# Performance work log

Measured on AMD Instinct MI355X. Metric: run time of the kernel, lower is better.

The kernel has to match this reference:

```python
import jax, jax.numpy as jnp
from jax import lax
import numpy as np


def conv2d(x, w, b=None, stride=1, pad=0, groups=1):
    out = lax.conv_general_dilated(x, w, (stride, stride), [(pad, pad), (pad, pad)],
                                   dimension_numbers=('NCHW', 'OIHW', 'NCHW'),
                                   feature_group_count=groups)
    if b is not None:
        out = out + b[None, :, None, None]
    return out


def ln(x, g, b, eps=1e-5):
    m = x.mean(-1, keepdims=True)
    v = ((x - m) ** 2).mean(-1, keepdims=True)
    return (x - m) * lax.rsqrt(v + eps) * g + b


def grid_sample_bilinear(img, grid):
    # img [N,C,H,W]; grid [N,Hg,Wg,2] with (x,y) in [-1,1]; align_corners=True, zeros padding
    N, C, H, W = img.shape
    x = (grid[..., 0] + 1.0) * 0.5 * (W - 1)
    y = (grid[..., 1] + 1.0) * 0.5 * (H - 1)
    x0 = jnp.floor(x); y0 = jnp.floor(y)
    x1 = x0 + 1.0; y1 = y0 + 1.0
    wx1 = x - x0; wx0 = 1.0 - wx1
    wy1 = y - y0; wy0 = 1.0 - wy1
    imgh = img.transpose(0, 2, 3, 1)  # [N,H,W,C]
    bidx = jnp.arange(N)[:, None, None]
    def g(ix, iy):
        valid = (ix >= 0) & (ix <= W - 1) & (iy >= 0) & (iy <= H - 1)
        ixc = jnp.clip(ix, 0, W - 1).astype(jnp.int32)
        iyc = jnp.clip(iy, 0, H - 1).astype(jnp.int32)
        return imgh[bidx, iyc, ixc] * valid[..., None].astype(img.dtype)
    out = (g(x0, y0) * (wx0 * wy0)[..., None] + g(x1, y0) * (wx1 * wy0)[..., None]
           + g(x0, y1) * (wx0 * wy1)[..., None] + g(x1, y1) * (wx1 * wy1)[..., None])
    return out.transpose(0, 3, 1, 2)  # [N,C,Hg,Wg]


def setup_inputs() -> dict:
    key = jax.random.key(0)
    ks = iter(jax.random.split(key, 64))
    def rn(shape, s=0.02):
        return jax.random.normal(next(ks), shape, jnp.float32) * s
    B, C, H, W = 4, 512, 32, 32
    gc, hid = 256, 1024
    d = {}
    d['feat_tgt'] = jax.random.normal(next(ks), (B, C, H, W), jnp.float32)
    d['feat_ref'] = jax.random.normal(next(ks), (B, C, H, W), jnp.float32)
    d['emb_w'] = rn((C, 2 * C, 3, 3)); d['emb_b'] = jnp.zeros((C,), jnp.float32)
    d['q_w'] = rn((C, C)); d['q_b'] = jnp.zeros((C,), jnp.float32)
    d['k_w'] = rn((C, C)); d['k_b'] = jnp.zeros((C,), jnp.float32)
    d['v_w'] = rn((C, C)); d['v_b'] = jnp.zeros((C,), jnp.float32)
    d['out_w'] = rn((C, C)); d['out_b'] = jnp.zeros((C,), jnp.float32)
    d['ln1_w'] = jnp.ones((gc,), jnp.float32); d['ln1_b'] = jnp.zeros((gc,), jnp.float32)
    d['mb_n1_w'] = jnp.ones((gc,), jnp.float32); d['mb_n1_b'] = jnp.zeros((gc,), jnp.float32)
    d['mb_q_w'] = rn((gc, gc)); d['mb_q_b'] = jnp.zeros((gc,), jnp.float32)
    d['mb_kv_w'] = rn((2 * gc, gc)); d['mb_kv_b'] = jnp.zeros((2 * gc,), jnp.float32)
    d['mb_proj_w'] = rn((gc, gc)); d['mb_proj_b'] = jnp.zeros((gc,), jnp.float32)
    d['mb_n2_w'] = jnp.ones((gc,), jnp.float32); d['mb_n2_b'] = jnp.zeros((gc,), jnp.float32)
    d['mb_fc1_w'] = rn((hid, gc)); d['mb_fc1_b'] = jnp.zeros((hid,), jnp.float32)
    d['mb_dw_w'] = rn((hid, 1, 3, 3)); d['mb_dw_b'] = jnp.zeros((hid,), jnp.float32)
    d['mb_fc2_w'] = rn((gc, hid)); d['mb_fc2_b'] = jnp.zeros((gc,), jnp.float32)
    d['co_dw_w'] = rn((gc, 1, 9, 9)); d['co_dw_b'] = jnp.zeros((gc,), jnp.float32)
    d['co_ln_w'] = jnp.ones((gc,), jnp.float32); d['co_ln_b'] = jnp.zeros((gc,), jnp.float32)
    d['co_out_w'] = rn((2, gc))
    return d


def reference(feat_tgt, feat_ref, emb_w, emb_b, q_w, q_b, k_w, k_b, v_w, v_b, out_w, out_b,
              ln1_w, ln1_b, mb_n1_w, mb_n1_b, mb_q_w, mb_q_b, mb_kv_w, mb_kv_b,
              mb_proj_w, mb_proj_b, mb_n2_w, mb_n2_b, mb_fc1_w, mb_fc1_b, mb_dw_w, mb_dw_b,
              mb_fc2_w, mb_fc2_b, co_dw_w, co_dw_b, co_ln_w, co_ln_b, co_out_w):
    B, C, H, W = feat_tgt.shape
    G = 2                      # n_groups
    gc = C // G                # n_group_channels
    heads, hc = 8, C // 8      # n_heads, n_head_channels
    # embedding conv over concat(target, reference)
    feat = conv2d(jnp.concatenate([feat_tgt, feat_ref], 1), emb_w, emb_b, pad=1)
    q = jnp.einsum('bchw,oc->bohw', feat_tgt, q_w) + q_b[None, :, None, None]
    # group tokens + LN
    fg = feat.reshape(B * G, gc, H * W).transpose(0, 2, 1)  # [BG, N, gc]
    x = ln(fg, ln1_w, ln1_b)
    # ---- MitBlock offset generator ----
    BG, N, D = x.shape
    mh = 8; mhd = D // mh
    h = ln(x, mb_n1_w, mb_n1_b, 1e-6)
    qq = (h @ mb_q_w.T + mb_q_b).reshape(BG, N, mh, mhd).transpose(0, 2, 1, 3)
    kv = (h @ mb_kv_w.T + mb_kv_b).reshape(BG, N, 2, mh, mhd).transpose(2, 0, 3, 1, 4)
    kk, vv = kv[0], kv[1]
    a = jax.nn.softmax(jnp.einsum('bhnd,bhmd->bhnm', qq, kk) * (mhd ** -0.5), axis=-1)
    o = jnp.einsum('bhnm,bhmd->bhnd', a, vv).transpose(0, 2, 1, 3).reshape(BG, N, D)
    x = x + (o @ mb_proj_w.T + mb_proj_b)
    h2 = ln(x, mb_n2_w, mb_n2_b, 1e-6)
    m = h2 @ mb_fc1_w.T + mb_fc1_b                         # [BG, N, hid]
    hid = m.shape[-1]
    mi = m.transpose(0, 2, 1).reshape(BG, hid, H, W)
    mi = conv2d(mi, mb_dw_w, mb_dw_b, pad=1, groups=hid)
    m = jax.nn.gelu(mi.reshape(BG, hid, N).transpose(0, 2, 1), approximate=False)
    x = x + (m @ mb_fc2_w.T + mb_fc2_b)
    # ---- conv_offset stack ----
    off = x.reshape(BG, H, W, gc).transpose(0, 3, 1, 2)
    off = conv2d(off, co_dw_w, co_dw_b, pad=4, groups=gc)
    off = ln(off.transpose(0, 2, 3, 1), co_ln_w, co_ln_b).transpose(0, 3, 1, 2)
    off = jax.nn.gelu(off, approximate=False)
    off = jnp.einsum('bchw,oc->bohw', off, co_out_w)       # [BG, 2, Hk, Wk]
    Hk, Wk = off.shape[2], off.shape[3]
    ns = Hk * Wk
    rng = jnp.array([1.0 / Hk, 1.0 / Wk], feat.dtype).reshape(1, 2, 1, 1)
    off = jnp.tanh(off) * rng * 2.0                        # offset_range_factor = 2
    off = off.transpose(0, 2, 3, 1)                        # [BG, Hk, Wk, 2] (y,x)
    ry = (jnp.linspace(0.5, Hk - 0.5, Hk, dtype=feat.dtype) / Hk) * 2 - 1
    rx = (jnp.linspace(0.5, Wk - 0.5, Wk, dtype=feat.dtype) / Wk) * 2 - 1
    ref = jnp.stack(jnp.meshgrid(ry, rx, indexing='ij'), -1)  # [Hk, Wk, 2] (y,x)
    pos = off + ref[None]
    sampled = grid_sample_bilinear(feat.reshape(BG, gc, H, W), pos[..., ::-1])
    sampled = sampled.reshape(B, C, ns)
    k = jnp.einsum('bcn,oc->bon', sampled, k_w) + k_b[None, :, None]
    v = jnp.einsum('bcn,oc->bon', sampled, v_w) + v_b[None, :, None]
    qh = q.reshape(B * heads, hc, H * W)
    kh = k.reshape(B * heads, hc, ns)
    vh = v.reshape(B * heads, hc, ns)
    attn = jax.nn.softmax(jnp.einsum('bcm,bcn->bmn', qh, kh) * (hc ** -0.5), axis=-1)
    out = jnp.einsum('bmn,bcn->bcm', attn, vh).reshape(B, C, H, W)
    y = jnp.einsum('bchw,oc->bohw', out, out_w) + out_b[None, :, None, None]
    return y
```

## Files before the change

### kernel.cpp

```cpp
#include <hip/hip_runtime.h>
#include <math.h>


static constexpr int HW = 1024;

typedef __attribute__((ext_vector_type(8))) short bf16x8;
typedef __attribute__((ext_vector_type(4))) float f32x4;

union V16u { int4 i4; ushort u[8]; };

__device__ __forceinline__ float gelu_exact(float v) {
  return 0.5f * v * (1.0f + erff(v * 0.7071067811865475f));
}

__device__ __forceinline__ ushort bf16_rne(float v) {
  unsigned int b = __float_as_uint(v);
  return (ushort)((b + 0x7fffu + ((b >> 16) & 1u)) >> 16);
}

__device__ __forceinline__ void split2(float v, ushort& h, ushort& l) {
  h = bf16_rne(v);
  l = bf16_rne(v - __uint_as_float(((unsigned int)h) << 16));
}

__device__ __forceinline__ void wfrag_body(const float* __restrict__ W, int K, int KC,
                                           ushort* __restrict__ dh, ushort* __restrict__ dl,
                                           int gtid) {
  int l = gtid & 63; int fr = gtid >> 6;
  int kc = fr % KC; int ot = fr / KC;
  int lr = l & 15, lu = l >> 4;
  const float* sp = W + (size_t)(ot * 16 + lr) * K + kc * 32 + lu * 8;
  V16u hi, lo;
#pragma unroll
  for (int j = 0; j < 8; ++j) split2(sp[j], hi.u[j], lo.u[j]);
  *(int4*)(dh + (size_t)gtid * 8) = hi.i4;
  *(int4*)(dl + (size_t)gtid * 8) = lo.i4;
}

__global__ void k_prep_all(
    const float* __restrict__ emb_w, const float* __restrict__ tgt,
    const float* __restrict__ refp,
    const float* q_w, const float* k_w, const float* v_w, const float* o_w,
    const float* mq_w, const float* mkv_w, const float* mp_w,
    const float* f1_w, const float* f2_w, const float* dw9_w,
    const float* mq_b, const float* mkv_b, const float* k_b, const float* v_b,
    ushort* __restrict__ WtEH, ushort* __restrict__ WtEL,
    ushort* __restrict__ XtH, ushort* __restrict__ XtL,
    ushort* qh, ushort* ql, ushort* kvh, ushort* kvl,
    ushort* oh, ushort* ol, ushort* mqkvh, ushort* mqkvl,
    ushort* mph, ushort* mpl, ushort* f1h, ushort* f1l, ushort* f2h, ushort* f2l,
    float* wt9, float* biasmb, float* biaskv) {
  int bid = blockIdx.x, tid = threadIdx.x;
  if (bid < 2048) {
    int idx = bid * 256 + tid;
    int o = idx >> 10, ci = idx & 1023;
    const float* src = emb_w + (size_t)idx * 9;
#pragma unroll
    for (int t = 0; t < 9; ++t) {
      ushort h, l; split2(src[t], h, l);
      size_t oo = ((size_t)(t * 512 + o)) * 1024 + ci;
      WtEH[oo] = h; WtEL[oo] = l;
    }
  } else if (bid < 4360) {
    int idx = (bid - 2048) * 256 + tid;
    int xp = idx % 34; int r = idx / 34;
    int g8 = r & 127; r >>= 7;
    int yp = r % 34; int b = r / 34;
    int y = yp - 1, x = xp - 1;
    bool valid = (unsigned)y < 32u && (unsigned)x < 32u;
    V16u hi, lo;
    const float* in = (g8 < 64) ? (tgt + ((size_t)(b * 512 + g8 * 8)) * HW)
                                : (refp + ((size_t)(b * 512 + (g8 - 64) * 8)) * HW);
#pragma unroll
    for (int j = 0; j < 8; ++j) {
      float v = valid ? in[(size_t)j * HW + y * 32 + x] : 0.f;
      split2(v, hi.u[j], lo.u[j]);
    }
    size_t oo = (((size_t)(b * 34 + yp)) * 34 + xp) * 1024 + g8 * 8;
    *(int4*)(XtH + oo) = hi.i4;
    *(int4*)(XtL + oo) = lo.i4;
  }
  else if (bid < 4488) wfrag_body(q_w, 512, 16, qh, ql, (bid - 4360) * 256 + tid);
  else if (bid < 4616) wfrag_body(k_w, 512, 16, kvh, kvl, (bid - 4488) * 256 + tid);
  else if (bid < 4744) wfrag_body(v_w, 512, 16, kvh + 262144, kvl + 262144,
                                  (bid - 4616) * 256 + tid);
  else if (bid < 4872) wfrag_body(o_w, 512, 16, oh, ol, (bid - 4744) * 256 + tid);
  else if (bid < 4904) wfrag_body(mq_w, 256, 8, mqkvh, mqkvl, (bid - 4872) * 256 + tid);
  else if (bid < 4968) wfrag_body(mkv_w, 256, 8, mqkvh + 65536, mqkvl + 65536,
                                  (bid - 4904) * 256 + tid);
  else if (bid < 5000) wfrag_body(mp_w, 256, 8, mph, mpl, (bid - 4968) * 256 + tid);
  else if (bid < 5128) wfrag_body(f1_w, 256, 8, f1h, f1l, (bid - 5000) * 256 + tid);
  else if (bid < 5256) wfrag_body(f2_w, 1024, 32, f2h, f2l, (bid - 5128) * 256 + tid);
  else if (bid < 5337) {
    int idx = (bid - 5256) * 256 + tid;
    int t = idx >> 8, c = idx & 255;
    wt9[idx] = dw9_w[c * 81 + t];
  } else {
    int idx = (bid - 5337) * 256 + tid;
    if (idx < 768) biasmb[idx] = idx < 256 ? mq_b[idx] : mkv_b[idx - 256];
    else if (idx < 1792) {
      int j = idx - 768;
      biaskv[j] = j < 512 ? k_b[j] : v_b[j - 512];
    }
  }
}

__global__ void k_prep_cm2frag(const float* __restrict__ src, int CH, int KC,
                               ushort* __restrict__ dh, ushort* __restrict__ dl) {
  int gtid = blockIdx.x * 256 + threadIdx.x;
  int l = gtid & 63; int fr = gtid >> 6;
  int kc = fr % KC; int r2 = fr / KC; int nt = r2 & 63; int b = r2 >> 6;
  int lr = l & 15, lu = l >> 4;
  const float* sp = src + ((size_t)(b * CH) + kc * 32 + lu * 8) * 1024 + nt * 16 + lr;
  V16u hi, lo;
#pragma unroll
  for (int j = 0; j < 8; ++j) split2(sp[(size_t)j * 1024], hi.u[j], lo.u[j]);
  *(int4*)(dh + (size_t)gtid * 8) = hi.i4;
  *(int4*)(dl + (size_t)gtid * 8) = lo.i4;
}

__global__ __launch_bounds__(256, 2)
void k_emb_mfma(const ushort* __restrict__ Xt_hi, const ushort* __restrict__ Xt_lo,
                const ushort* __restrict__ Wt_hi, const ushort* __restrict__ Wt_lo,
                float* __restrict__ part) {
  int wgid = (blockIdx.x & 7) * 64 + (blockIdx.x >> 3);
  int yt = wgid & 7;  wgid >>= 3;
  int b  = wgid & 3;  wgid >>= 2;
  int mt = wgid & 3;  wgid >>= 2;
  int ks = wgid;
  int tid = threadIdx.x;
  int w = tid >> 6, l = tid & 63;
  int lr = l & 15, lu = l >> 4;
  int y0 = yt * 4;
  int obase = mt * 128 + w * 32;

  __shared__ int4 LsH[2][816];
  __shared__ int4 LsL[2][816];

  int4 gh[4], gl[4];
  int kc0 = ks * 8;

  auto loadstage = [&](int kcg) {
#pragma unroll
    for (int i = 0; i < 4; ++i) {
      int s = tid + 256 * i;
      if (s < 816) {
        int px = s >> 2;
        int u = (s & 3) ^ ((px >> 1) & 3);
        size_t off = ((size_t)(b * 34 + y0) * 34 + px) * 1024 + kcg * 32 + u * 8;
        gh[i] = *(const int4*)(Xt_hi + off);
        gl[i] = *(const int4*)(Xt_lo + off);
      }
    }
  };
  auto writestage = [&](int buf) {
// ... 112 lines not shown
void k_gemm_mfma(const ushort* __restrict__ Ah, const ushort* __restrict__ Al,
                 const ushort* __restrict__ Bh, const ushort* __restrict__ Bl,
                 const float* __restrict__ bias, float* __restrict__ Y,
                 int KC, int MT, int Mtot) {
  int bid = blockIdx.x;
  int ntb = bid & 15; bid >>= 4;
  int mt = bid % MT; int b = bid / MT;
  int tid = threadIdx.x, w = tid >> 6, l = tid & 63, lr = l & 15, lu = l >> 4;
  int wo = w >> 1, wn = w & 1;
  int ot0 = mt * 4 + wo * 2;
  int nf0 = ntb * 4 + wn * 2;
  const bf16x8* pAh = (const bf16x8*)Ah;
  const bf16x8* pAl = (const bf16x8*)Al;
  const bf16x8* pBh = (const bf16x8*)Bh;
  const bf16x8* pBl = (const bf16x8*)Bl;
  f32x4 zero = {0.f, 0.f, 0.f, 0.f};
  f32x4 acc[2][2];
#pragma unroll
  for (int a = 0; a < 2; ++a)
#pragma unroll
    for (int n = 0; n < 2; ++n) acc[a][n] = zero;
  for (int kc = 0; kc < KC; ++kc) {
    bf16x8 a_h[2], a_l[2];
#pragma unroll
    for (int a = 0; a < 2; ++a) {
      size_t idx = ((size_t)(ot0 + a) * KC + kc) * 64 + l;
      a_h[a] = pAh[idx]; a_l[a] = pAl[idx];
    }
#pragma unroll
    for (int n = 0; n < 2; ++n) {
      size_t idx = (((size_t)(b * 64 + nf0 + n)) * KC + kc) * 64 + l;
      bf16x8 b_h = pBh[idx], b_l = pBl[idx];
#pragma unroll
      for (int a = 0; a < 2; ++a) {
        acc[a][n] = __builtin_amdgcn_mfma_f32_16x16x32_bf16(a_h[a], b_h, acc[a][n], 0, 0, 0);
        acc[a][n] = __builtin_amdgcn_mfma_f32_16x16x32_bf16(a_h[a], b_l, acc[a][n], 0, 0, 0);
        acc[a][n] = __builtin_amdgcn_mfma_f32_16x16x32_bf16(a_l[a], b_h, acc[a][n], 0, 0, 0);
      }
    }
  }
#pragma unroll
  for (int a = 0; a < 2; ++a) {
    int o = (ot0 + a) * 16 + lu * 4;
#pragma unroll
    for (int n = 0; n < 2; ++n) {
      int col = (nf0 + n) * 16 + lr;
#pragma unroll
      for (int r = 0; r < 4; ++r)
        Y[((size_t)(b * Mtot + o + r)) * 1024 + col] = acc[a][n][r] + bias[o + r];
    }
  }
}

__global__ void k_transadd_tm(const float* __restrict__ Pcm, float* __restrict__ Xtm) {
  __shared__ float T[64][65];
  int bid = blockIdx.x; int n0 = (bid & 15) << 6; bid >>= 4;
  int c0 = (bid & 3) << 6; int bg = bid >> 2;
  int cl = threadIdx.x & 63, rw = threadIdx.x >> 6;
#pragma unroll
  for (int i = 0; i < 16; ++i) {
    int crow = i * 4 + rw;
    T[crow][cl] = Pcm[((size_t)(bg * 256 + c0 + crow)) * 1024 + n0 + cl];
  }
  __syncthreads();
#pragma unroll
  for (int i = 0; i < 16; ++i) {
    int nrow = i * 4 + rw;
    Xtm[((size_t)((bg << 10) + n0 + nrow)) * 256 + c0 + cl] += T[cl][nrow];
  }
}

__global__ void k_transadd_nc(const float* __restrict__ Yg, const float* __restrict__ Xtm,
                              float* __restrict__ out_nc) {
  __shared__ float T[64][65];
  int bid = blockIdx.x; int n0 = (bid & 15) << 6; bid >>= 4;
  int c0 = (bid & 3) << 6; int bg = bid >> 2;
  int cl = threadIdx.x & 63, rw = threadIdx.x >> 6;
#pragma unroll
  for (int i = 0; i < 16; ++i) {
    int crow = i * 4 + rw;
    T[crow][cl] = Yg[((size_t)(bg * 256 + c0 + crow)) * 1024 + n0 + cl];
  }
  __syncthreads();
#pragma unroll
  for (int i = 0; i < 16; ++i) {
    int nrow = i * 4 + rw;
    size_t a = ((size_t)((bg << 10) + n0 + nrow)) * 256 + c0 + cl;
    out_nc[a] = T[cl][nrow] + Xtm[a];
  }
}

__global__ void k_ln1n1(const float* __restrict__ featnc,
                        const float* __restrict__ g1, const float* __restrict__ b1,
                        const float* __restrict__ gn, const float* __restrict__ bn,
                        float* __restrict__ xbuf,
                        ushort* __restrict__ dh, ushort* __restrict__ dl) {
  int token = (blockIdx.x * 256 + threadIdx.x) >> 6;
  int lane = threadIdx.x & 63;
  float4 v4 = *reinterpret_cast<const float4*>(featnc + (size_t)token * 256 + lane * 4);
  float s  = v4.x + v4.y + v4.z + v4.w;
  float s2 = v4.x * v4.x + v4.y * v4.y + v4.z * v4.z + v4.w * v4.w;
#pragma unroll
  for (int off = 32; off; off >>= 1) { s += __shfl_xor(s, off); s2 += __shfl_xor(s2, off); }
  float mean = s * (1.f / 256.f);
  float rstd = rsqrtf(s2 * (1.f / 256.f) - mean * mean + 1e-5f);
  float4 g4 = *reinterpret_cast<const float4*>(g1 + lane * 4);
  float4 b4 = *reinterpret_cast<const float4*>(b1 + lane * 4);
  float4 x;
  x.x = (v4.x - mean) * rstd * g4.x + b4.x;
  x.y = (v4.y - mean) * rstd * g4.y + b4.y;
  x.z = (v4.z - mean) * rstd * g4.z + b4.z;
  x.w = (v4.w - mean) * rstd * g4.w + b4.w;
  *reinterpret_cast<float4*>(xbuf + (size_t)token * 256 + lane * 4) = x;
  float t  = x.x + x.y + x.z + x.w;
  float t2 = x.x * x.x + x.y * x.y + x.z * x.z + x.w * x.w;
#pragma unroll
  for (int off = 32; off; off >>= 1) { t += __shfl_xor(t, off); t2 += __shfl_xor(t2, off); }
  float mean2 = t * (1.f / 256.f);
  float rstd2 = rsqrtf(t2 * (1.f / 256.f) - mean2 * mean2 + 1e-6f);
  float4 gg = *reinterpret_cast<const float4*>(gn + lane * 4);
  float4 bb = *reinterpret_cast<const float4*>(bn + lane * 4);
  ushort4 h4, l4;
  split2((x.x - mean2) * rstd2 * gg.x + bb.x, h4.x, l4.x);
  split2((x.y - mean2) * rstd2 * gg.y + bb.y, h4.y, l4.y);
  split2((x.z - mean2) * rstd2 * gg.z + bb.z, h4.z, l4.z);
  split2((x.w - mean2) * rstd2 * gg.w + bb.w, h4.w, l4.w);
  int bg = token >> 10, nt = (token >> 4) & 63, lr = token & 15;
  int kc = lane >> 3, lu_f = (lane >> 1) & 3, j0 = (lane & 1) * 4;
  size_t base = ((((size_t)(bg * 64 + nt)) * 8 + kc) * 64 + lu_f * 16 + lr) * 8 + j0;
  *(ushort4*)(dh + base) = h4;
  *(ushort4*)(dl + base) = l4;
}

__global__ void k_ln_frag(const float* __restrict__ xin, const float* __restrict__ g_,
                          const float* __restrict__ b_, ushort* __restrict__ dh,
                          ushort* __restrict__ dl, float eps) {
  int token = (blockIdx.x * 256 + threadIdx.x) >> 6;
  int lane = threadIdx.x & 63;
  float4 v4 = *reinterpret_cast<const float4*>(xin + (size_t)token * 256 + lane * 4);
  float s  = v4.x + v4.y + v4.z + v4.w;
  float s2 = v4.x * v4.x + v4.y * v4.y + v4.z * v4.z + v4.w * v4.w;
#pragma unroll
  for (int off = 32; off; off >>= 1) { s += __shfl_xor(s, off); s2 += __shfl_xor(s2, off); }
  float mean = s * (1.f / 256.f);
  float rstd = rsqrtf(s2 * (1.f / 256.f) - mean * mean + eps);
  float4 g4 = *reinterpret_cast<const float4*>(g_ + lane * 4);
  float4 b4 = *reinterpret_cast<const float4*>(b_ + lane * 4);
  ushort4 h4, l4;
  split2((v4.x - mean) * rstd * g4.x + b4.x, h4.x, l4.x);
  split2((v4.y - mean) * rstd * g4.y + b4.y, h4.y, l4.y);
  split2((v4.z - mean) * rstd * g4.z + b4.z, h4.z, l4.z);
  split2((v4.w - mean) * rstd * g4.w + b4.w, h4.w, l4.w);
  int bg = token >> 10, nt = (token >> 4) & 63, lr = token & 15;
  int kc = lane >> 3, lu_f = (lane >> 1) & 3, j0 = (lane & 1) * 4;
  size_t base = ((((size_t)(bg * 64 + nt)) * 8 + kc) * 64 + lu_f * 16 + lr) * 8 + j0;
  *(ushort4*)(dh + base) = h4;
  *(ushort4*)(dl + base) = l4;
}

__global__ void k_prep_mb3(const float* __restrict__ qkv,
                           ushort* __restrict__ mQh, ushort* __restrict__ mQl,
                           ushort* __restrict__ mKh, ushort* __restrict__ mKl,
                           ushort* __restrict__ mVh, ushort* __restrict__ mVl) {
  int bid = blockIdx.x, tid = threadIdx.x;
  int sect = bid >> 10, lb = bid & 1023;
  int gtid = lb * 256 + tid;
  int l = gtid & 63; int fr = gtid >> 6;
  int lr = l & 15, lu = l >> 4;
  V16u hi, lo;
  if (sect < 2) {
    int nt = fr & 63; int bgh = fr >> 6;
    int bg = bgh >> 3, hh = bgh & 7;
    int rowbase = sect == 0 ? 0 : 256;
    float scale = sect == 0 ? 0.17677669529663689f : 1.f;
    const float* sp = qkv + ((size_t)(bg * 768 + rowbase + hh * 32 + lu * 8)) * 1024
                      + nt * 16 + lr;
#pragma unroll
    for (int j = 0; j < 8; ++j) split2(sp[(size_t)j * 1024] * scale, hi.u[j], lo.u[j]);
    ushort* dh = sect == 0 ? mQh : mKh;
    ushort* dl = sect == 0 ? mQl : mKl;
    *(int4*)(dh + (size_t)gtid * 8) = hi.i4;
    *(int4*)(dl + (size_t)gtid * 8) = lo.i4;
  } else {
    int kc = fr & 31; int et = (fr >> 5) & 1; int bgh = fr >> 6;
    int bg = bgh >> 3, hh = bgh & 7;
    const float* sp = qkv + ((size_t)(bg * 768 + 512 + hh * 32 + et * 16 + lr)) * 1024
                      + kc * 32 + lu * 8;
#pragma unroll
    for (int j = 0; j < 8; ++j) split2(sp[j], hi.u[j], lo.u[j]);
    *(int4*)(mVh + (size_t)gtid * 8) = hi.i4;
    *(int4*)(mVl + (size_t)gtid * 8) = lo.i4;
  }
}

__global__ void k_prep_main3(const float* __restrict__ qb, const float* __restrict__ kv2,
                             ushort* __restrict__ aQh, ushort* __restrict__ aQl,
                             ushort* __restrict__ aKh, ushort* __restrict__ aKl,
                             ushort* __restrict__ aVh, ushort* __restrict__ aVl) {
  int bid = blockIdx.x, tid = threadIdx.x;
  int sect = bid >> 10, lb = bid & 1023;
  int gtid = lb * 256 + tid;
  int l = gtid & 63, tile = gtid >> 6;
  int lr = l & 15, lu = l >> 4;
  V16u hi, lo;
  if (sect < 2) {
    int dc = tile & 1, nt = (tile >> 1) & 63, bh = tile >> 7;
    int b = bh >> 3, h = bh & 7;
    const float* sp;
    float scale;
    if (sect == 0) {
      scale = 0.125f;
      sp = qb + ((size_t)(b * 512 + h * 64 + dc * 32 + lu * 8)) * 1024 + nt * 16 + lr;
    } else {
      scale = 1.f;
      sp = kv2 + ((size_t)(b * 1024 + h * 64 + dc * 32 + lu * 8)) * 1024 + nt * 16 + lr;
    }
#pragma unroll
    for (int j = 0; j < 8; ++j) split2(sp[(size_t)j * 1024] * scale, hi.u[j], lo.u[j]);
    ushort* dh = sect == 0 ? aQh : aKh;
    ushort* dl = sect == 0 ? aQl : aKl;
    *(int4*)(dh + (size_t)gtid * 8) = hi.i4;
    *(int4*)(dl + (size_t)gtid * 8) = lo.i4;
  } else {
    int kc = tile & 31, et = (tile >> 5) & 3, bh = tile >> 7;
    int b = bh >> 3, h = bh & 7;
    const float* sp = kv2 + ((size_t)(b * 1024 + 512 + h * 64 + et * 16 + lr)) * 1024
                      + kc * 32 + lu * 8;
#pragma unroll
    for (int j = 0; j < 8; ++j) split2(sp[j], hi.u[j], lo.u[j]);
    *(int4*)(aVh + (size_t)gtid * 8) = hi.i4;
    *(int4*)(aVl + (size_t)gtid * 8) = lo.i4;
  }
}

__global__ __launch_bounds__(256)
void k_mbattn_mfma(const ushort* __restrict__ Qh, const ushort* __restrict__ Ql,
                   const ushort* __restrict__ Kh, const ushort* __restrict__ Kl,
                   const ushort* __restrict__ Vh, const ushort* __restrict__ Vl,
                   ushort* __restrict__ ofh, ushort* __restrict__ ofl) {
  int qb = blockIdx.x & 15, bgh = blockIdx.x >> 4;
  int tid = threadIdx.x, w = tid >> 6, l = tid & 63, lr = l & 15, lu = l >> 4;
  int qt = qb * 4 + w;
  bf16x8 qh = ((const bf16x8*)Qh)[(size_t)(bgh * 64 + qt) * 64 + l];
  bf16x8 ql = ((const bf16x8*)Ql)[(size_t)(bgh * 64 + qt) * 64 + l];
  __shared__ ushort Ph[4][16][72];
  __shared__ ushort Pl[4][16][72];
  f32x4 zero = {0.f, 0.f, 0.f, 0.f};
  f32x4 oacc[2] = {zero, zero};
  float den = 0.f;
  for (int kb = 0; kb < 16; ++kb) {
#pragma unroll
    for (int kt4 = 0; kt4 < 4; ++kt4) {
      int kt = kb * 4 + kt4;
      bf16x8 kh = ((const bf16x8*)Kh)[(size_t)(bgh * 64 + kt) * 64 + l];
      bf16x8 kl = ((const bf16x8*)Kl)[(size_t)(bgh * 64 + kt) * 64 + l];
      f32x4 s = zero;
      s = __builtin_amdgcn_mfma_f32_16x16x32_bf16(kh, qh, s, 0, 0, 0);
      s = __builtin_amdgcn_mfma_f32_16x16x32_bf16(kh, ql, s, 0, 0, 0);
      s = __builtin_amdgcn_mfma_f32_16x16x32_bf16(kl, qh, s, 0, 0, 0);
      uint2 uh, ul;
      {
        float p0 = __expf(s[0]), p1 = __expf(s[1]), p2 = __expf(s[2]), p3 = __expf(s[3]);
        den += (p0 + p1) + (p2 + p3);
        ushort h0, l0, h1, l1, h2, l2, h3, l3;
        split2(p0, h0, l0); split2(p1, h1, l1); split2(p2, h2, l2); split2(p3, h3, l3);
        uh.x = (unsigned)h0 | ((unsigned)h1 << 16); uh.y = (unsigned)h2 | ((unsigned)h3 << 16);
        ul.x = (unsigned)l0 | ((unsigned)l1 << 16); ul.y = (unsigned)l2 | ((unsigned)l3 << 16);
      }
      *(uint2*)&Ph[w][lr][kt4 * 16 + lu * 4] = uh;
      *(uint2*)&Pl[w][lr][kt4 * 16 + lu * 4] = ul;
    }
#pragma unroll
    for (int kc2 = 0; kc2 < 2; ++kc2) {
      int kc = kb * 2 + kc2;
      bf16x8 bph = *(const bf16x8*)&Ph[w][lr][kc2 * 32 + lu * 8];
      bf16x8 bpl = *(const bf16x8*)&Pl[w][lr][kc2 * 32 + lu * 8];
#pragma unroll
      for (int et = 0; et < 2; ++et) {
        bf16x8 vh = ((const bf16x8*)Vh)[(size_t)((bgh * 2 + et) * 32 + kc) * 64 + l];
        bf16x8 vl = ((const bf16x8*)Vl)[(size_t)((bgh * 2 + et) * 32 + kc) * 64 + l];
        oacc[et] = __builtin_amdgcn_mfma_f32_16x16x32_bf16(vh, bph, oacc[et], 0, 0, 0);
        oacc[et] = __builtin_amdgcn_mfma_f32_16x16x32_bf16(vh, bpl, oacc[et], 0, 0, 0);
        oacc[et] = __builtin_amdgcn_mfma_f32_16x16x32_bf16(vl, bph, oacc[et], 0, 0, 0);
      }
    }
// ... 210 lines not shown
  }
  __syncthreads();
  const float* src = Xnc + (size_t)(bg << 10) * 256;
  for (int n = 0; n < 64; ++n) {
    float acc = src[(size_t)sI[0][n] * 256 + tid] * sW[0][n]
              + src[(size_t)sI[1][n] * 256 + tid] * sW[1][n]
              + src[(size_t)sI[2][n] * 256 + tid] * sW[2][n]
              + src[(size_t)sI[3][n] * 256 + tid] * sW[3][n];
    out_nc[((size_t)((bg << 10) + nch * 64 + n)) * 256 + tid] = acc;
  }
}

extern "C" void kernel_launch(void* const* d_in, const int* in_sizes, int n_in,
                              void* d_out, int out_size, void* d_ws, size_t ws_size,
                              hipStream_t stream) {
  const float* tgt    = (const float*)d_in[0];
  const float* refp   = (const float*)d_in[1];
  const float* emb_w  = (const float*)d_in[2];
  const float* emb_b  = (const float*)d_in[3];
  const float* q_w    = (const float*)d_in[4];
  const float* q_b    = (const float*)d_in[5];
  const float* k_w    = (const float*)d_in[6];
  const float* k_b    = (const float*)d_in[7];
  const float* v_w    = (const float*)d_in[8];
  const float* v_b    = (const float*)d_in[9];
  const float* out_w  = (const float*)d_in[10];
  const float* out_b  = (const float*)d_in[11];
  const float* ln1_w  = (const float*)d_in[12];
  const float* ln1_b  = (const float*)d_in[13];
  const float* n1_w   = (const float*)d_in[14];
  const float* n1_b   = (const float*)d_in[15];
  const float* mbq_w  = (const float*)d_in[16];
  const float* mbq_b  = (const float*)d_in[17];
  const float* mbkv_w = (const float*)d_in[18];
  const float* mbkv_b = (const float*)d_in[19];
  const float* mbp_w  = (const float*)d_in[20];
  const float* mbp_b  = (const float*)d_in[21];
  const float* n2_w   = (const float*)d_in[22];
  const float* n2_b   = (const float*)d_in[23];
  const float* fc1_w  = (const float*)d_in[24];
  const float* fc1_b  = (const float*)d_in[25];
  const float* dw3_w  = (const float*)d_in[26];
  const float* dw3_b  = (const float*)d_in[27];
  const float* fc2_w  = (const float*)d_in[28];
  const float* fc2_b  = (const float*)d_in[29];
  const float* dw9_w  = (const float*)d_in[30];
  const float* dw9_b  = (const float*)d_in[31];
  const float* coln_w = (const float*)d_in[32];
  const float* coln_b = (const float*)d_in[33];
  const float* coout_w= (const float*)d_in[34];

  float* ws = (float*)d_ws;
  float* slabA = ws + 0;
  float* qbuf  = ws + 2097152;
  float* xbuf  = ws + 4194304;
  float* slabD = ws + 6291456;
  float* slabE = ws + 8388608;
  float* slabF = ws + 10485760;
  float* slabG = ws + 14680064;
  float* slabH = ws + 23068672;
  float* featnc= ws + 31457280;
  float* posb  = ws + 35389440;
  float* wt9   = ws + 35405824;
  float* biasmb= ws + 35426560;
  float* biaskv= ws + 35427328;

  ushort* XtH = (ushort*)(ws + 4194304);
  ushort* XtL = XtH + 4734976;
  ushort* WtEH = (ushort*)slabG;
  ushort* WtEL = WtEH + 4718592;
  float* part = slabH;
  ushort* tgtfh = (ushort*)slabF;
  ushort* tgtfl = tgtfh + 2097152;

  ushort* J = (ushort*)(ws + 33554432);
  ushort* wfq_h   = J;                ushort* wfq_l   = J + 262144;
  ushort* wfkv_h  = J + 524288;       ushort* wfkv_l  = J + 1048576;
  ushort* wfo_h   = J + 1572864;      ushort* wfo_l   = J + 1835008;
  ushort* wfmqkv_h= J + 2097152;      ushort* wfmqkv_l= J + 2293760;
  ushort* wfmp_h  = J + 2490368;      ushort* wfmp_l  = J + 2555904;
  ushort* wff1_h  = J + 2621440;      ushort* wff1_l  = J + 2883584;
  ushort* wff2_h  = J + 3145728;      ushort* wff2_l  = J + 3407872;

  ushort* hfh = (ushort*)slabG;     ushort* hfl = hfh + 2097152;
  float* qkv_cm = slabE;
  ushort* mQh = (ushort*)slabG;     ushort* mQl = mQh + 2097152;
  ushort* mKh = mQh + 4194304;      ushort* mKl = mQh + 6291456;
  ushort* mVh = mQh + 8388608;      ushort* mVl = mQh + 10485760;
  ushort* ofh = (ushort*)slabF;     ushort* ofl = ofh + 2097152;
  float* P_cm = slabD;
  ushort* h2fh = (ushort*)slabF;    ushort* h2fl = h2fh + 2097152;
  float* m_cm = slabG;
  float* mi_cm = slabH;
  ushort* mifh = (ushort*)slabG;    ushort* mifl = mifh + 8388608;
  float* ygemm = slabD;
  float* offin = slabA;
  float* offdwnc = slabE;
  float* samplednc = slabA;
  ushort* sfh = (ushort*)slabF;     ushort* sfl = sfh + 2097152;
  float* kv2 = slabD;
  ushort* aQh = (ushort*)slabG;     ushort* aQl = aQh + 2097152;
  ushort* aKh = aQh + 4194304;      ushort* aKl = aQh + 6291456;
  ushort* aVh = aQh + 8388608;      ushort* aVl = aQh + 10485760;
  ushort* anfh = (ushort*)slabH;    ushort* anfl = anfh + 2097152;

  k_prep_all<<<5344, 256, 0, stream>>>(
      emb_w, tgt, refp, q_w, k_w, v_w, out_w, mbq_w, mbkv_w, mbp_w, fc1_w, fc2_w,
      dw9_w, mbq_b, mbkv_b, k_b, v_b,
      WtEH, WtEL, XtH, XtL,
      wfq_h, wfq_l, wfkv_h, wfkv_l, wfo_h, wfo_l, wfmqkv_h, wfmqkv_l,
      wfmp_h, wfmp_l, wff1_h, wff1_l, wff2_h, wff2_l,
      wt9, biasmb, biaskv);
  k_prep_cm2frag<<<1024, 256, 0, stream>>>(tgt, 512, 16, tgtfh, tgtfl);
  k_emb_mfma<<<512, 256, 0, stream>>>(XtH, XtL, WtEH, WtEL, part);
  k_embmerge_nc<<<512, 256, 0, stream>>>(part, emb_b, featnc);
  k_gemm_mfma<<<512, 256, 0, stream>>>(wfq_h, wfq_l, tgtfh, tgtfl, q_b, qbuf, 16, 8, 512);
  k_ln1n1<<<2048, 256, 0, stream>>>(featnc, ln1_w, ln1_b, n1_w, n1_b, xbuf, hfh, hfl);
  k_gemm_mfma<<<1536, 256, 0, stream>>>(wfmqkv_h, wfmqkv_l, hfh, hfl, biasmb, qkv_cm, 8, 12, 768);
  k_prep_mb3<<<3072, 256, 0, stream>>>(qkv_cm, mQh, mQl, mKh, mKl, mVh, mVl);
  k_mbattn_mfma<<<1024, 256, 0, stream>>>(mQh, mQl, mKh, mKl, mVh, mVl, ofh, ofl);
  k_gemm_mfma<<<512, 256, 0, stream>>>(wfmp_h, wfmp_l, ofh, ofl, mbp_b, P_cm, 8, 4, 256);
  k_transadd_tm<<<512, 256, 0, stream>>>(P_cm, xbuf);
  k_ln_frag<<<2048, 256, 0, stream>>>(xbuf, n2_w, n2_b, h2fh, h2fl, 1e-6f);
  k_gemm_mfma<<<2048, 256, 0, stream>>>(wff1_h, wff1_l, h2fh, h2fl, fc1_b, m_cm, 8, 16, 1024);
  k_dw3<<<32768, 256, 0, stream>>>(m_cm, dw3_w, dw3_b, mi_cm);
  k_prep_cm2frag<<<4096, 256, 0, stream>>>(mi_cm, 1024, 32, mifh, mifl);
  k_gemm_mfma<<<512, 256, 0, stream>>>(wff2_h, wff2_l, mifh, mifl, fc2_b, ygemm, 32, 4, 256);
  k_transadd_nc<<<512, 256, 0, stream>>>(ygemm, xbuf, offin);
  k_dw9_nc<<<1024, 256, 0, stream>>>(offin, wt9, dw9_b, offdwnc);
  k_cotail_nc<<<2048, 256, 0, stream>>>(offdwnc, coln_w, coln_b, coout_w, posb);
  k_gsample_nc<<<128, 256, 0, stream>>>(featnc, posb, samplednc);
  k_prep_s2frag<<<1024, 256, 0, stream>>>(samplednc, sfh, sfl);
  k_gemm_mfma<<<1024, 256, 0, stream>>>(wfkv_h, wfkv_l, sfh, sfl, biaskv, kv2, 16, 16, 1024);
  k_prep_main3<<<3072, 256, 0, stream>>>(qbuf, kv2, aQh, aQl, aKh, aKl, aVh, aVl);
  k_mainattn_mfma<<<512, 256, 0, stream>>>(aQh, aQl, aKh, aKl, aVh, aVl, anfh, anfl);
  k_gemm_mfma<<<512, 256, 0, stream>>>(wfo_h, wfo_l, anfh, anfl, out_b, (float*)d_out, 16, 8, 512);
}
```

Before: 591.5 us.

## Fuse Q/K/V fragment packing into GEMM epilogues and fold attention scale into weights

Result: faster. 575.7 us (-2.7%).

```diff
diff --git a/kernel.cpp b/kernel.cpp
--- a/kernel.cpp
+++ b/kernel.cpp
@@ -25,14 +25,14 @@
 
 __device__ __forceinline__ void wfrag_body(const float* __restrict__ W, int K, int KC,
                                            ushort* __restrict__ dh, ushort* __restrict__ dl,
-                                           int gtid) {
+                                           int gtid, float scale) {
   int l = gtid & 63; int fr = gtid >> 6;
   int kc = fr % KC; int ot = fr / KC;
   int lr = l & 15, lu = l >> 4;
   const float* sp = W + (size_t)(ot * 16 + lr) * K + kc * 32 + lu * 8;
   V16u hi, lo;
 #pragma unroll
-  for (int j = 0; j < 8; ++j) split2(sp[j], hi.u[j], lo.u[j]);
+  for (int j = 0; j < 8; ++j) split2(sp[j] * scale, hi.u[j], lo.u[j]);
   *(int4*)(dh + (size_t)gtid * 8) = hi.i4;
   *(int4*)(dl + (size_t)gtid * 8) = lo.i4;
 }
@@ -43,13 +43,14 @@
     const float* q_w, const float* k_w, const float* v_w, const float* o_w,
     const float* mq_w, const float* mkv_w, const float* mp_w,
     const float* f1_w, const float* f2_w, const float* dw9_w,
-    const float* mq_b, const float* mkv_b, const float* k_b, const float* v_b,
+    const float* q_b, const float* mq_b, const float* mkv_b,
+    const float* k_b, const float* v_b,
     ushort* __restrict__ WtEH, ushort* __restrict__ WtEL,
     ushort* __restrict__ XtH, ushort* __restrict__ XtL,
     ushort* qh, ushort* ql, ushort* kvh, ushort* kvl,
     ushort* oh, ushort* ol, ushort* mqkvh, ushort* mqkvl,
     ushort* mph, ushort* mpl, ushort* f1h, ushort* f1l, ushort* f2h, ushort* f2l,
-    float* wt9, float* biasmb, float* biaskv) {
+    float* wt9, float* biasmb, float* biaskv, float* biasq) {
   int bid = blockIdx.x, tid = threadIdx.x;
   if (bid < 2048) {
     int idx = bid * 256 + tid;
@@ -80,27 +81,31 @@
     *(int4*)(XtH + oo) = hi.i4;
     *(int4*)(XtL + oo) = lo.i4;
   }
-  else if (bid < 4488) wfrag_body(q_w, 512, 16, qh, ql, (bid - 4360) * 256 + tid);
-  else if (bid < 4616) wfrag_body(k_w, 512, 16, kvh, kvl, (bid - 4488) * 256 + tid);
+  else if (bid < 4488) wfrag_body(q_w, 512, 16, qh, ql, (bid - 4360) * 256 + tid, 0.125f);
+  else if (bid < 4616) wfrag_body(k_w, 512, 16, kvh, kvl, (bid - 4488) * 256 + tid, 1.f);
   else if (bid < 4744) wfrag_body(v_w, 512, 16, kvh + 262144, kvl + 262144,
-                                  (bid - 4616) * 256 + tid);
-  else if (bid < 4872) wfrag_body(o_w, 512, 16, oh, ol, (bid - 4744) * 256 + tid);
-  else if (bid < 4904) wfrag_body(mq_w, 256, 8, mqkvh, mqkvl, (bid - 4872) * 256 + tid);
+                                  (bid - 4616) * 256 + tid, 1.f);
+  else if (bid < 4872) wfrag_body(o_w, 512, 16, oh, ol, (bid - 4744) * 256 + tid, 1.f);
+  else if (bid < 4904) wfrag_body(mq_w, 256, 8, mqkvh, mqkvl, (bid - 4872) * 256 + tid,
+                                  0.17677669529663689f);
   else if (bid < 4968) wfrag_body(mkv_w, 256, 8, mqkvh + 65536, mqkvl + 65536,
-                                  (bid - 4904) * 256 + tid);
-  else if (bid < 5000) wfrag_body(mp_w, 256, 8, mph, mpl, (bid - 4968) * 256 + tid);
-  else if (bid < 5128) wfrag_body(f1_w, 256, 8, f1h, f1l, (bid - 5000) * 256 + tid);
-  else if (bid < 5256) wfrag_body(f2_w, 1024, 32, f2h, f2l, (bid - 5128) * 256 + tid);
+                                  (bid - 4904) * 256 + tid, 1.f);
+  else if (bid < 5000) wfrag_body(mp_w, 256, 8, mph, mpl, (bid - 4968) * 256 + tid, 1.f);
+  else if (bid < 5128) wfrag_body(f1_w, 256, 8, f1h, f1l, (bid - 5000) * 256 + tid, 1.f);
+  else if (bid < 5256) wfrag_body(f2_w, 1024, 32, f2h, f2l, (bid - 5128) * 256 + tid, 1.f);
   else if (bid < 5337) {
     int idx = (bid - 5256) * 256 + tid;
     int t = idx >> 8, c = idx & 255;
     wt9[idx] = dw9_w[c * 81 + t];
   } else {
     int idx = (bid - 5337) * 256 + tid;
-    if (idx < 768) biasmb[idx] = idx < 256 ? mq_b[idx] : mkv_b[idx - 256];
+    if (idx < 768)
+      biasmb[idx] = idx < 256 ? mq_b[idx] * 0.17677669529663689f : mkv_b[idx - 256];
     else if (idx < 1792) {
       int j = idx - 768;
       biaskv[j] = j < 512 ? k_b[j] : v_b[j - 512];
+    } else if (idx < 2304) {
+      biasq[idx - 1792] = q_b[idx - 1792] * 0.125f;
     }
   }
 }
@@ -319,6 +324,156 @@
   }
 }
 
+__global__ __launch_bounds__(256)
+void k_gemm_frag_mb(const ushort* __restrict__ Ah, const ushort* __restrict__ Al,
+                    const ushort* __restrict__ Bh, const ushort* __restrict__ Bl,
+                    const float* __restrict__ bias,
+                    ushort* __restrict__ mQh, ushort* __restrict__ mQl,
+                    ushort* __restrict__ mKh, ushort* __restrict__ mKl,
+                    ushort* __restrict__ mVh, ushort* __restrict__ mVl) {
+  int bid = blockIdx.x;
+  int ntb = bid & 15; bid >>= 4;
+  int mt = bid % 12; int b = bid / 12;
+  int tid = threadIdx.x, w = tid >> 6, l = tid & 63, lr = l & 15, lu = l >> 4;
+  int wo = w >> 1, wn = w & 1;
+  int ot0 = mt * 4 + wo * 2;
+  int nf0 = ntb * 4 + wn * 2;
+  const bf16x8* pAh = (const bf16x8*)Ah;
+  const bf16x8* pAl = (const bf16x8*)Al;
+  const bf16x8* pBh = (const bf16x8*)Bh;
+  const bf16x8* pBl = (const bf16x8*)Bl;
+  f32x4 zero = {0.f, 0.f, 0.f, 0.f};
+  f32x4 acc[2][2];
+#pragma unroll
+  for (int a = 0; a < 2; ++a)
+#pragma unroll
+    for (int n = 0; n < 2; ++n) acc[a][n] = zero;
+  for (int kc = 0; kc < 8; ++kc) {
+    bf16x8 a_h[2], a_l[2];
+#pragma unroll
+    for (int a = 0; a < 2; ++a) {
+      size_t idx = ((size_t)(ot0 + a) * 8 + kc) * 64 + l;
+      a_h[a] = pAh[idx]; a_l[a] = pAl[idx];
+    }
+#pragma unroll
+    for (int n = 0; n < 2; ++n) {
+      size_t idx = (((size_t)(b * 64 + nf0 + n)) * 8 + kc) * 64 + l;
+      bf16x8 b_h = pBh[idx], b_l = pBl[idx];
+#pragma unroll
+      for (int a = 0; a < 2; ++a) {
+        acc[a][n] = __builtin_amdgcn_mfma_f32_16x16x32_bf16(a_h[a], b_h, acc[a][n], 0, 0, 0);
+        acc[a][n] = __builtin_amdgcn_mfma_f32_16x16x32_bf16(a_h[a], b_l, acc[a][n], 0, 0, 0);
+        acc[a][n] = __builtin_amdgcn_mfma_f32_16x16x32_bf16(a_l[a], b_h, acc[a][n], 0, 0, 0);
+      }
+    }
+  }
+#pragma unroll
+  for (int a = 0; a < 2; ++a) {
+    int o0 = (ot0 + a) * 16 + lu * 4;
+#pragma unroll
+    for (int n = 0; n < 2; ++n) {
+      int col = (nf0 + n) * 16 + lr;
+      ushort4 h4, l4;
+      split2(acc[a][n][0] + bias[o0 + 0], h4.x, l4.x);
+      split2(acc[a][n][1] + bias[o0 + 1], h4.y, l4.y);
+      split2(acc[a][n][2] + bias[o0 + 2], h4.z, l4.z);
+      split2(acc[a][n][3] + bias[o0 + 3], h4.w, l4.w);
+      if (o0 < 512) {
+        int oo = o0 & 255;
+        int hh = oo >> 5, d = oo & 31;
+        ushort* dh = o0 < 256 ? mQh : mKh;
+        ushort* dl = o0 < 256 ? mQl : mKl;
+        size_t base = ((((size_t)(b * 8 + hh) * 64 + (col >> 4)) * 64)
+                       + ((d >> 3) << 4) + (col & 15)) * 8 + (d & 7);
+        *(ushort4*)(dh + base) = h4;
+        *(ushort4*)(dl + base) = l4;
+      } else {
+        int oo = o0 - 512;
+        int hh = oo >> 5, d = oo & 31;
+        int et = d >> 4;
+        size_t eb = ((((size_t)((b * 8 + hh) * 2 + et)) * 32 + (col >> 5)) * 64
+                     + ((col >> 3) & 3) * 16 + (d & 15)) * 8 + (col & 7);
+        mVh[eb] = h4.x; mVh[eb + 8] = h4.y; mVh[eb + 16] = h4.z; mVh[eb + 24] = h4.w;
+        mVl[eb] = l4.x; mVl[eb + 8] = l4.y; mVl[eb + 16] = l4.z; mVl[eb + 24] = l4.w;
+      }
+    }
+  }
+}
+
+__global__ __launch_bounds__(256)
+void k_gemm_frag_main(const ushort* __restrict__ Ah, const ushort* __restrict__ Al,
+                      const ushort* __restrict__ Bh, const ushort* __restrict__ Bl,
+                      const float* __restrict__ bias,
+                      ushort* __restrict__ fh, ushort* __restrict__ fl,
+                      ushort* __restrict__ vfh, ushort* __restrict__ vfl,
+                      int vbase, int KC, int MT) {
+  int bid = blockIdx.x;
+  int ntb = bid & 15; bid >>= 4;
+  int mt = bid % MT; int b = bid / MT;
+  int tid = threadIdx.x, w = tid >> 6, l = tid & 63, lr = l & 15, lu = l >> 4;
+  int wo = w >> 1, wn = w & 1;
+  int ot0 = mt * 4 + wo * 2;
+  int nf0 = ntb * 4 + wn * 2;
+  const bf16x8* pAh = (const bf16x8*)Ah;
+  const bf16x8* pAl = (const bf16x8*)Al;
+  const bf16x8* pBh = (const bf16x8*)Bh;
+  const bf16x8* pBl = (const bf16x8*)Bl;
+  f32x4 zero = {0.f, 0.f, 0.f, 0.f};
+  f32x4 acc[2][2];
+#pragma unroll
+  for (int a = 0; a < 2; ++a)
+#pragma unroll
+    for (int n = 0; n < 2; ++n) acc[a][n] = zero;
+  for (int kc = 0; kc < KC; ++kc) {
+    bf16x8 a_h[2], a_l[2];
+#pragma unroll
+    for (int a = 0; a < 2; ++a) {
+      size_t idx = ((size_t)(ot0 + a) * KC + kc) * 64 + l;
+      a_h[a] = pAh[idx]; a_l[a] = pAl[idx];
+    }
+#pragma unroll
+    for (int n = 0; n < 2; ++n) {
+      size_t idx = (((size_t)(b * 64 + nf0 + n)) * KC + kc) * 64 + l;
+      bf16x8 b_h = pBh[idx], b_l = pBl[idx];
+#pragma unroll
+      for (int a = 0; a < 2; ++a) {
+        acc[a][n] = __builtin_amdgcn_mfma_f32_16x16x32_bf16(a_h[a], b_h, acc[a][n], 0, 0, 0);
+        acc[a][n] = __builtin_amdgcn_mfma_f32_16x16x32_bf16(a_h[a], b_l, acc[a][n], 0, 0, 0);
+        acc[a][n] = __builtin_amdgcn_mfma_f32_16x16x32_bf16(a_l[a], b_h, acc[a][n], 0, 0, 0);
+      }
+    }
+  }
+#pragma unroll
+  for (int a = 0; a < 2; ++a) {
+    int o0 = (ot0 + a) * 16 + lu * 4;
+#pragma unroll
+    for (int n = 0; n < 2; ++n) {
+      int col = (nf0 + n) * 16 + lr;
+      ushort4 h4, l4;
+      split2(acc[a][n][0] + bias[o0 + 0], h4.x, l4.x);
+      split2(acc[a][n][1] + bias[o0 + 1], h4.y, l4.y);
+      split2(acc[a][n][2] + bias[o0 + 2], h4.z, l4.z);
+      split2(acc[a][n][3] + bias[o0 + 3], h4.w, l4.w);
+      if (o0 < vbase) {
+        int h = o0 >> 6, d = o0 & 63;
+        int dc = d >> 5;
+        size_t base = (((((size_t)(b * 8 + h) * 64 + (col >> 4)) * 2 + dc) * 64)
+                       + (((d & 31) >> 3) << 4) + (col & 15)) * 8 + (d & 7);
+        *(ushort4*)(fh + base) = h4;
+        *(ushort4*)(fl + base) = l4;
+      } else {
+        int oo = o0 - vbase;
+        int h = oo >> 6, d = oo & 63;
+        int et = d >> 4;
+        size_t eb = ((((size_t)((b * 8 + h) * 4 + et)) * 32 + (col >> 5)) * 64
+                     + ((col >> 3) & 3) * 16 + (d & 15)) * 8 + (col & 7);
+        vfh[eb] = h4.x; vfh[eb + 8] = h4.y; vfh[eb + 16] = h4.z; vfh[eb + 24] = h4.w;
+        vfl[eb] = l4.x; vfl[eb + 8] = l4.y; vfl[eb + 16] = l4.z; vfl[eb + 24] = l4.w;
+      }
+    }
+  }
+}
+
 __global__ void k_transadd_tm(const float* __restrict__ Pcm, float* __restrict__ Xtm) {
   __shared__ float T[64][65];
   int bid = blockIdx.x; int n0 = (bid & 15) << 6; bid >>= 4;
@@ -423,81 +578,6 @@
   size_t base = ((((size_t)(bg * 64 + nt)) * 8 + kc) * 64 + lu_f * 16 + lr) * 8 + j0;
   *(ushort4*)(dh + base) = h4;
   *(ushort4*)(dl + base) = l4;
-}
-
-__global__ void k_prep_mb3(const float* __restrict__ qkv,
-                           ushort* __restrict__ mQh, ushort* __restrict__ mQl,
-                           ushort* __restrict__ mKh, ushort* __restrict__ mKl,
-                           ushort* __restrict__ mVh, ushort* __restrict__ mVl) {
-  int bid = blockIdx.x, tid = threadIdx.x;
-  int sect = bid >> 10, lb = bid & 1023;
-  int gtid = lb * 256 + tid;
-  int l = gtid & 63; int fr = gtid >> 6;
-  int lr = l & 15, lu = l >> 4;
-  V16u hi, lo;
-  if (sect < 2) {
-    int nt = fr & 63; int bgh = fr >> 6;
-    int bg = bgh >> 3, hh = bgh & 7;
-    int rowbase = sect == 0 ? 0 : 256;
-    float scale = sect == 0 ? 0.17677669529663689f : 1.f;
-    const float* sp = qkv + ((size_t)(bg * 768 + rowbase + hh * 32 + lu * 8)) * 1024
-                      + nt * 16 + lr;
-#pragma unroll
-    for (int j = 0; j < 8; ++j) split2(sp[(size_t)j * 1024] * scale, hi.u[j], lo.u[j]);
-    ushort* dh = sect == 0 ? mQh : mKh;
-    ushort* dl = sect == 0 ? mQl : mKl;
-    *(int4*)(dh + (size_t)gtid * 8) = hi.i4;
-    *(int4*)(dl + (size_t)gtid * 8) = lo.i4;
-  } else {
-    int kc = fr & 31; int et = (fr >> 5) & 1; int bgh = fr >> 6;
-    int bg = bgh >> 3, hh = bgh & 7;
-    const float* sp = qkv + ((size_t)(bg * 768 + 512 + hh * 32 + et * 16 + lr)) * 1024
-                      + kc * 32 + lu * 8;
-#pragma unroll
-    for (int j = 0; j < 8; ++j) split2(sp[j], hi.u[j], lo.u[j]);
-    *(int4*)(mVh + (size_t)gtid * 8) = hi.i4;
-    *(int4*)(mVl + (size_t)gtid * 8) = lo.i4;
-  }
-}
-
-__global__ void k_prep_main3(const float* __restrict__ qb, const float* __restrict__ kv2,
-                             ushort* __restrict__ aQh, ushort* __restrict__ aQl,
-                             ushort* __restrict__ aKh, ushort* __restrict__ aKl,
-                             ushort* __restrict__ aVh, ushort* __restrict__ aVl) {
-  int bid = blockIdx.x, tid = threadIdx.x;
-  int sect = bid >> 10, lb = bid & 1023;
-  int gtid = lb * 256 + tid;
-  int l = gtid & 63, tile = gtid >> 6;
-  int lr = l & 15, lu = l >> 4;
-  V16u hi, lo;
-  if (sect < 2) {
-    int dc = tile & 1, nt = (tile >> 1) & 63, bh = tile >> 7;
-    int b = bh >> 3, h = bh & 7;
-    const float* sp;
-    float scale;
-    if (sect == 0) {
-      scale = 0.125f;
-      sp = qb + ((size_t)(b * 512 + h * 64 + dc * 32 + lu * 8)) * 1024 + nt * 16 + lr;
-    } else {
-      scale = 1.f;
-      sp = kv2 + ((size_t)(b * 1024 + h * 64 + dc * 32 + lu * 8)) * 1024 + nt * 16 + lr;
-    }
-#pragma unroll
-    for (int j = 0; j < 8; ++j) split2(sp[(size_t)j * 1024] * scale, hi.u[j], lo.u[j]);
-    ushort* dh = sect == 0 ? aQh : aKh;
-    ushort* dl = sect == 0 ? aQl : aKl;
-    *(int4*)(dh + (size_t)gtid * 8) = hi.i4;
-    *(int4*)(dl + (size_t)gtid * 8) = lo.i4;
-  } else {
-    int kc = tile & 31, et = (tile >> 5) & 3, bh = tile >> 7;
-    int b = bh >> 3, h = bh & 7;
-    const float* sp = kv2 + ((size_t)(b * 1024 + 512 + h * 64 + et * 16 + lr)) * 1024
-                      + kc * 32 + lu * 8;
-#pragma unroll
-    for (int j = 0; j < 8; ++j) split2(sp[j], hi.u[j], lo.u[j]);
-    *(int4*)(aVh + (size_t)gtid * 8) = hi.i4;
-    *(int4*)(aVl + (size_t)gtid * 8) = lo.i4;
-  }
 }
 
 __global__ __launch_bounds__(256)
@@ -814,7 +894,7 @@
 
   float* ws = (float*)d_ws;
   float* slabA = ws + 0;
-  float* qbuf  = ws + 2097152;
+  float* qfrag = ws + 2097152;
   float* xbuf  = ws + 4194304;
   float* slabD = ws + 6291456;
   float* slabE = ws + 8388608;
@@ -826,6 +906,7 @@
   float* wt9   = ws + 35405824;
   float* biasmb= ws + 35426560;
   float* biaskv= ws + 35427328;
+  float* biasq = ws + 35428352;
 
   ushort* XtH = (ushort*)(ws + 4194304);
   ushort* XtL = XtH + 4734976;
@@ -844,8 +925,7 @@
   ushort* wff1_h  = J + 2621440;      ushort* wff1_l  = J + 2883584;
   ushort* wff2_h  = J + 3145728;      ushort* wff2_l  = J + 3407872;
 
-  ushort* hfh = (ushort*)slabG;     ushort* hfl = hfh + 2097152;
-  float* qkv_cm = slabE;
+  ushort* hfh = (ushort*)slabH;     ushort* hfl = hfh + 2097152;
   ushort* mQh = (ushort*)slabG;     ushort* mQl = mQh + 2097152;
   ushort* mKh = mQh + 4194304;      ushort* mKl = mQh + 6291456;
   ushort* mVh = mQh + 8388608;      ushort* mVl = mQh + 10485760;
@@ -860,26 +940,26 @@
   float* offdwnc = slabE;
   float* samplednc = slabA;
   ushort* sfh = (ushort*)slabF;     ushort* sfl = sfh + 2097152;
-  float* kv2 = slabD;
-  ushort* aQh = (ushort*)slabG;     ushort* aQl = aQh + 2097152;
-  ushort* aKh = aQh + 4194304;      ushort* aKl = aQh + 6291456;
-  ushort* aVh = aQh + 8388608;      ushort* aVl = aQh + 10485760;
+  ushort* aQh = (ushort*)qfrag;     ushort* aQl = aQh + 2097152;
+  ushort* aKh = (ushort*)slabG;     ushort* aKl = aKh + 2097152;
+  ushort* aVh = aKh + 4194304;      ushort* aVl = aKh + 6291456;
   ushort* anfh = (ushort*)slabH;    ushort* anfl = anfh + 2097152;
 
-  k_prep_all<<<5344, 256, 0, stream>>>(
+  k_prep_all<<<5346, 256, 0, stream>>>(
       emb_w, tgt, refp, q_w, k_w, v_w, out_w, mbq_w, mbkv_w, mbp_w, fc1_w, fc2_w,
-      dw9_w, mbq_b, mbkv_b, k_b, v_b,
+      dw9_w, q_b, mbq_b, mbkv_b, k_b, v_b,
       WtEH, WtEL, XtH, XtL,
       wfq_h, wfq_l, wfkv_h, wfkv_l, wfo_h, wfo_l, wfmqkv_h, wfmqkv_l,
       wfmp_h, wfmp_l, wff1_h, wff1_l, wff2_h, wff2_l,
-      wt9, biasmb, biaskv);
+      wt9, biasmb, biaskv, biasq);
   k_prep_cm2frag<<<1024, 256, 0, stream>>>(tgt, 512, 16, tgtfh, tgtfl);
   k_emb_mfma<<<512, 256, 0, stream>>>(XtH, XtL, WtEH, WtEL, part);
   k_embmerge_nc<<<512, 256, 0, stream>>>(part, emb_b, featnc);
-  k_gemm_mfma<<<512, 256, 0, stream>>>(wfq_h, wfq_l, tgtfh, tgtfl, q_b, qbuf, 16, 8, 512);
+  k_gemm_frag_main<<<512, 256, 0, stream>>>(wfq_h, wfq_l, tgtfh, tgtfl, biasq,
+                                            aQh, aQl, aVh, aVl, 512, 16, 8);
   k_ln1n1<<<2048, 256, 0, stream>>>(featnc, ln1_w, ln1_b, n1_w, n1_b, xbuf, hfh, hfl);
-  k_gemm_mfma<<<1536, 256, 0, stream>>>(wfmqkv_h, wfmqkv_l, hfh, hfl, biasmb, qkv_cm, 8, 12, 768);
-  k_prep_mb3<<<3072, 256, 0, stream>>>(qkv_cm, mQh, mQl, mKh, mKl, mVh, mVl);
+  k_gemm_frag_mb<<<1536, 256, 0, stream>>>(wfmqkv_h, wfmqkv_l, hfh, hfl, biasmb,
+                                           mQh, mQl, mKh, mKl, mVh, mVl);
   k_mbattn_mfma<<<1024, 256, 0, stream>>>(mQh, mQl, mKh, mKl, mVh, mVl, ofh, ofl);
   k_gemm_mfma<<<512, 256, 0, stream>>>(wfmp_h, wfmp_l, ofh, ofl, mbp_b, P_cm, 8, 4, 256);
   k_transadd_tm<<<512, 256, 0, stream>>>(P_cm, xbuf);
@@ -893,8 +973,8 @@
   k_cotail_nc<<<2048, 256, 0, stream>>>(offdwnc, coln_w, coln_b, coout_w, posb);
   k_gsample_nc<<<128, 256, 0, stream>>>(featnc, posb, samplednc);
   k_prep_s2frag<<<1024, 256, 0, stream>>>(samplednc, sfh, sfl);
-  k_gemm_mfma<<<1024, 256, 0, stream>>>(wfkv_h, wfkv_l, sfh, sfl, biaskv, kv2, 16, 16, 1024);
-  k_prep_main3<<<3072, 256, 0, stream>>>(qbuf, kv2, aQh, aQl, aKh, aKl, aVh, aVl);
+  k_gemm_frag_main<<<1024, 256, 0, stream>>>(wfkv_h, wfkv_l, sfh, sfl, biaskv,
+                                             aKh, aKl, aVh, aVl, 512, 16, 16);
   k_mainattn_mfma<<<512, 256, 0, stream>>>(aQh, aQl, aKh, aKl, aVh, aVl, anfh, anfl);
   k_gemm_mfma<<<512, 256, 0, stream>>>(wfo_h, wfo_l, anfh, anfl, out_b, (float*)d_out, 16, 8, 512);
 }
```
